# Performance work log

Hardware: AMD Instinct MI355X
Metric: run time of the kernel (lower is better)

Reference implementation:

```python
import jax, jax.numpy as jnp
import numpy as np

N = 50000
E = 800000
IN_CH = 128
HID = 32
HEADS = 4
OUT_CH = 64
NEG_SLOPE = 0.2


def _gat_conv(x, src, dst, W, att_src, att_dst, bias, heads, out_ch, concat):
    # x: [N, F_in]; W: [F_in, heads*out_ch]; att_*: [heads, out_ch]; bias: [heads*out_ch] or [out_ch]
    n = x.shape[0]
    h = (x @ W).reshape(n, heads, out_ch)                  # [N, H, C]
    a_src = jnp.einsum('nhc,hc->nh', h, att_src)           # [N, H]
    a_dst = jnp.einsum('nhc,hc->nh', h, att_dst)           # [N, H]
    alpha = jax.nn.leaky_relu(a_src[src] + a_dst[dst], NEG_SLOPE)  # [E, H]
    # segment softmax over edges grouped by destination node
    amax = jax.ops.segment_max(alpha, dst, num_segments=n)  # [N, H]
    ex = jnp.exp(alpha - amax[dst])
    denom = jax.ops.segment_sum(ex, dst, num_segments=n)    # [N, H]
    att = ex / (denom[dst] + 1e-16)                         # [E, H]
    msg = h[src] * att[:, :, None]                          # [E, H, C]
    out = jax.ops.segment_sum(msg, dst, num_segments=n)     # [N, H, C]
    out = out.reshape(n, heads * out_ch) if concat else out.mean(axis=1)
    return out + bias


def setup_inputs() -> dict:
    key = jax.random.key(0)
    ks = jax.random.split(key, 9)
    x = jax.random.normal(ks[0], (N, IN_CH), dtype=jnp.float32)
    edge_index = jax.random.randint(ks[1], (2, E), 0, N, dtype=jnp.int64)
    s = 1.0 / np.sqrt(IN_CH)
    W1 = jax.random.normal(ks[2], (IN_CH, HEADS * HID), dtype=jnp.float32) * s
    att_src1 = jax.random.normal(ks[3], (HEADS, HID), dtype=jnp.float32) * 0.1
    att_dst1 = jax.random.normal(ks[4], (HEADS, HID), dtype=jnp.float32) * 0.1
    b1 = jnp.zeros((HEADS * HID,), dtype=jnp.float32)
    s2 = 1.0 / np.sqrt(HEADS * HID)
    W2 = jax.random.normal(ks[5], (HEADS * HID, OUT_CH), dtype=jnp.float32) * s2
    att_src2 = jax.random.normal(ks[6], (1, OUT_CH), dtype=jnp.float32) * 0.1
    att_dst2 = jax.random.normal(ks[7], (1, OUT_CH), dtype=jnp.float32) * 0.1
    b2 = jnp.zeros((OUT_CH,), dtype=jnp.float32)
    return {"x": x, "edge_index": edge_index, "W1": W1, "att_src1": att_src1,
            "att_dst1": att_dst1, "b1": b1, "W2": W2, "att_src2": att_src2,
            "att_dst2": att_dst2, "b2": b2}


def reference(x, edge_index, W1, att_src1, att_dst1, b1, W2, att_src2, att_dst2, b2):
    n = x.shape[0]
    # add self loops (PyG GATConv default add_self_loops=True)
    loops = jnp.arange(n, dtype=edge_index.dtype)
    src = jnp.concatenate([edge_index[0], loops])
    dst = jnp.concatenate([edge_index[1], loops])
    h = _gat_conv(x, src, dst, W1, att_src1, att_dst1, b1, HEADS, HID, True)
    h = jax.nn.leaky_relu(h, NEG_SLOPE)
    # dropout p=0.6 is identity at eval
    out = _gat_conv(h, src, dst, W2, att_src2, att_dst2, b2, 1, OUT_CH, False)
    return out
```

## Files before the change

### kernel.cpp

```cpp
#include <hip/hip_runtime.h>
#include <hip/hip_fp16.h>

#define NNODES 50000
#define NEDGES 800000
#define NSLOPE 0.2f
#define NB2 782
#define BCAP2 1280
#define CSRB 256
#define EPB 3125
#define PAH 136

typedef _Float16 half8v __attribute__((ext_vector_type(8)));
typedef float floatx4 __attribute__((ext_vector_type(4)));

__device__ __forceinline__ float lrelu(float x) { return x > 0.f ? x : NSLOPE * x; }

__device__ __forceinline__ void fmamix8(float* acc, uint4 v, float w) {
    asm("v_fma_mix_f32 %0, %1, %2, %0 op_sel:[0,0,0] op_sel_hi:[0,1,0]" : "+v"(acc[0]) : "v"(w), "v"(v.x));
    asm("v_fma_mix_f32 %0, %1, %2, %0 op_sel:[0,1,0] op_sel_hi:[0,1,0]" : "+v"(acc[1]) : "v"(w), "v"(v.x));
    asm("v_fma_mix_f32 %0, %1, %2, %0 op_sel:[0,0,0] op_sel_hi:[0,1,0]" : "+v"(acc[2]) : "v"(w), "v"(v.y));
    asm("v_fma_mix_f32 %0, %1, %2, %0 op_sel:[0,1,0] op_sel_hi:[0,1,0]" : "+v"(acc[3]) : "v"(w), "v"(v.y));
    asm("v_fma_mix_f32 %0, %1, %2, %0 op_sel:[0,0,0] op_sel_hi:[0,1,0]" : "+v"(acc[4]) : "v"(w), "v"(v.z));
    asm("v_fma_mix_f32 %0, %1, %2, %0 op_sel:[0,1,0] op_sel_hi:[0,1,0]" : "+v"(acc[5]) : "v"(w), "v"(v.z));
    asm("v_fma_mix_f32 %0, %1, %2, %0 op_sel:[0,0,0] op_sel_hi:[0,1,0]" : "+v"(acc[6]) : "v"(w), "v"(v.w));
    asm("v_fma_mix_f32 %0, %1, %2, %0 op_sel:[0,1,0] op_sel_hi:[0,1,0]" : "+v"(acc[7]) : "v"(w), "v"(v.w));
}

__global__ __launch_bounds__(256) void wconv_kernel(const float* __restrict__ W1,
                                                    const float* __restrict__ W2,
                                                    __half* __restrict__ Wf1,
                                                    __half* __restrict__ Wf2) {
    int tid = blockIdx.x * 256 + threadIdx.x;
    if (tid < 2048) {
        int l = tid & 63, t = (tid >> 6) & 7, ks = tid >> 9;
        int col = t * 16 + (l & 15), kq = l >> 4;
        __half* dst = Wf1 + (size_t)tid * 8;
#pragma unroll
        for (int j = 0; j < 8; j++)
            dst[j] = __float2half(W1[(ks * 32 + kq * 8 + j) * 128 + col]);
    } else if (tid < 3072) {
        int u = tid - 2048;
        int l = u & 63, t = (u >> 6) & 3, ks = u >> 8;
        int col = t * 16 + (l & 15), kq = l >> 4;
        __half* dst = Wf2 + (size_t)u * 8;
#pragma unroll
        for (int j = 0; j < 8; j++)
            dst[j] = __float2half(W2[(ks * 32 + kq * 8 + j) * 64 + col]);
    }
}

template<int NCOL, int HEADS, typename AT>
__device__ void gemm_mfma_body(int bid, __half* __restrict__ Ah,
                               const AT* __restrict__ A, const __half* __restrict__ Wf,
                               const float* __restrict__ atts, const float* __restrict__ attd,
                               __half* __restrict__ H, float* __restrict__ as_,
                               float* __restrict__ ad_, int nrows) {
    constexpr int NT = NCOL / 16;
    constexpr int TPH = NT / HEADS;
    int t = threadIdx.x;
    long r0 = (long)bid * 64;
    long abase = r0 * 128, alimit = (long)nrows * 128;
#pragma unroll
    for (int i = 0; i < 8; i++) {
        int off = i * 1024 + t * 4;
        uint2 pk = make_uint2(0, 0);
        if (abase + off < alimit) {
            if constexpr (sizeof(AT) == 4) {
                float4 v = *(const float4*)&A[abase + off];
                __half2 h0 = __floats2half2_rn(v.x, v.y);
                __half2 h1 = __floats2half2_rn(v.z, v.w);
                pk = make_uint2(*(unsigned*)&h0, *(unsigned*)&h1);
            } else {
                pk = *(const uint2*)&A[abase + off];
            }
        }
        *(uint2*)&Ah[(off >> 7) * PAH + (off & 127)] = pk;
    }
    __syncthreads();

    int w = t >> 6, l = t & 63;
    int i16 = l & 15, q = l >> 4;
    floatx4 acc[NT];
#pragma unroll
    for (int n = 0; n < NT; n++) acc[n] = (floatx4)0.f;
    const half8v* wf = (const half8v*)Wf;
#pragma unroll
    for (int ks = 0; ks < 4; ks++) {
        half8v afrag = *(const half8v*)&Ah[(w * 16 + i16) * PAH + ks * 32 + q * 8];
#pragma unroll
        for (int n = 0; n < NT; n++) {
            half8v bfrag = wf[(ks * NT + n) * 64 + l];
            acc[n] = __builtin_amdgcn_mfma_f32_16x16x32_f16(afrag, bfrag, acc[n], 0, 0, 0);
        }
    }
    long rb = r0 + w * 16 + q * 4;
#pragma unroll
    for (int n = 0; n < NT; n++) {
#pragma unroll
        for (int reg = 0; reg < 4; reg++) {
            long row = rb + reg;
            if (row < nrows) H[row * NCOL + n * 16 + i16] = __float2half(acc[n][reg]);
        }
    }
    float ps[4][HEADS], pd[4][HEADS];
#pragma unroll
    for (int reg = 0; reg < 4; reg++)
#pragma unroll
        for (int h = 0; h < HEADS; h++) { ps[reg][h] = 0.f; pd[reg][h] = 0.f; }
#pragma unroll
    for (int n = 0; n < NT; n++) {
        float sa = atts[n * 16 + i16], da = attd[n * 16 + i16];
        int h = n / TPH;
#pragma unroll
        for (int reg = 0; reg < 4; reg++) {
            ps[reg][h] += acc[n][reg] * sa;
            pd[reg][h] += acc[n][reg] * da;
        }
    }
#pragma unroll
    for (int reg = 0; reg < 4; reg++)
#pragma unroll
        for (int h = 0; h < HEADS; h++)
#pragma unroll
            for (int m = 1; m < 16; m <<= 1) {
                ps[reg][h] += __shfl_xor(ps[reg][h], m);
                pd[reg][h] += __shfl_xor(pd[reg][h], m);
            }
    if (i16 < HEADS) {
        int h = i16;
#pragma unroll
        for (int reg = 0; reg < 4; reg++) {
            long row = rb + reg;
            if (row < nrows) {
                float pv = 0.f, dv = 0.f;
#pragma unroll
                for (int hh = 0; hh < HEADS; hh++) { if (hh == h) { pv = ps[reg][hh]; dv = pd[reg][hh]; } }
                as_[row * HEADS + h] = pv;
                ad_[row * HEADS + h] = dv;
            }
        }
    }
}

__global__ __launch_bounds__(256) void fused_csr_gemm1_kernel(
    const int* __restrict__ ei, unsigned* __restrict__ priv,
    int* __restrict__ cnt_mtx, int* __restrict__ lofs_mtx,
    const float* __restrict__ A, const __half* __restrict__ Wf1,
    const float* __restrict__ atts, const float* __restrict__ attd,
    __half* __restrict__ H, float* __restrict__ as_, float* __restrict__ ad_, int nrows) {
    __shared__ __align__(16) char smem[21760];
    if (blockIdx.x >= CSRB) {
        gemm_mfma_body<128, 4, float>(blockIdx.x - CSRB, (__half*)smem, A, Wf1, atts, attd,
                                      H, as_, ad_, nrows);
        return;
    }
    int* hist = (int*)smem;
    int* lofs = hist + 1024;
    int* sbuf = lofs + 1024;
    unsigned* ebuf = (unsigned*)(sbuf + 256);
    int tid = threadIdx.x;
    for (int i = tid; i < 1024; i += 256) hist[i] = 0;
    __syncthreads();
    int e0 = blockIdx.x * EPB;
    int dreg[13];
#pragma unroll
    for (int i = 0; i < 13; i++) {
        int e = e0 + i * 256 + tid;
        dreg[i] = (e < e0 + EPB) ? ei[NEDGES + e] : -1;
        if (dreg[i] >= 0) atomicAdd(&hist[dreg[i] >> 6], 1);
    }
    __syncthreads();
    int t4 = tid * 4;
    int a0 = hist[t4], a1 = hist[t4 + 1], a2 = hist[t4 + 2], a3 = hist[t4 + 3];
    int p1 = a0 + a1, p2 = p1 + a2, p3 = p2 + a3;
    sbuf[tid] = p3;
    __syncthreads();
    for (int off = 1; off < 256; off <<= 1) {
        int v = (tid >= off) ? sbuf[tid - off] : 0;
        __syncthreads();
        sbuf[tid] += v;
        __syncthreads();
    }
    int base = (tid > 0) ? sbuf[tid - 1] : 0;
    lofs[t4] = base; lofs[t4 + 1] = base + a0; lofs[t4 + 2] = base + p1; lofs[t4 + 3] = base + p2;
#pragma unroll
    for (int j = 0; j < 4; j++) {
        int i = t4 + j;
        if (i < NB2) {
            cnt_mtx[(long)blockIdx.x * NB2 + i] = hist[i];
            lofs_mtx[(long)blockIdx.x * NB2 + i] = lofs[i];
        }
    }
    hist[t4] = 0; hist[t4 + 1] = 0; hist[t4 + 2] = 0; hist[t4 + 3] = 0;
    __syncthreads();
#pragma unroll
    for (int i = 0; i < 13; i++) {
        if (dreg[i] >= 0) {
            int e = e0 + i * 256 + tid;
            int s = ei[e];
            int b = dreg[i] >> 6;
            int r = atomicAdd(&hist[b], 1);
            ebuf[lofs[b] + r] = (unsigned)s | ((unsigned)(dreg[i] & 63) << 16);
        }
    }
    __syncthreads();
    unsigned* seg = priv + (long)blockIdx.x * EPB;
    for (int i = tid; i < EPB; i += 256) seg[i] = ebuf[i];
}

__global__ __launch_bounds__(256) void consumer_kernel(
    const unsigned* __restrict__ priv, const int* __restrict__ cnt_mtx,
    const int* __restrict__ lofs_mtx, int* __restrict__ ssrc,
    int* __restrict__ offs, int* __restrict__ ends) {
    __shared__ int dcnt[64], dbase[64], dcur[64];
    __shared__ unsigned ebuf[BCAP2];
    int b = blockIdx.x, tid = threadIdx.x;
    if (tid < 64) dcnt[tid] = 0;
    int cnt = cnt_mtx[(long)tid * NB2 + b];
    int lof = lofs_mtx[(long)tid * NB2 + b];
    const unsigned* seg = priv + (long)tid * EPB + lof;
    __syncthreads();
    for (int k = 0; k < cnt; k++) {
        unsigned v = seg[k];
        atomicAdd(&dcnt[(v >> 16) & 63], 1);
    }
    __syncthreads();
    if (tid < 64) {
        int v = dcnt[tid], p = v;
#pragma unroll
        for (int off = 1; off < 64; off <<= 1) {
            int u = __shfl_up(p, off);
            if (tid >= off) p += u;
        }
        dbase[tid] = p - v;
        dcur[tid] = p - v;
    }
    __syncthreads();
    for (int k = 0; k < cnt; k++) {
        unsigned v = seg[k];
        int dl = (v >> 16) & 63;
        int r = atomicAdd(&dcur[dl], 1);
        if (r < BCAP2) ebuf[r] = v & 0xFFFFu;
    }
    __syncthreads();
    int obase = b * BCAP2;
    int n = dbase[63] + dcnt[63];
    if (n > BCAP2) n = BCAP2;
    for (int i = tid; i < n; i += 256) ssrc[obase + i] = (int)ebuf[i];
    if (tid < 64) {
        int d = b * 64 + tid;
        if (d < NNODES) {
            int s0 = dbase[tid], e1 = s0 + dcnt[tid];
            if (s0 > BCAP2) s0 = BCAP2;
            if (e1 > BCAP2) e1 = BCAP2;
            offs[d] = obase + s0;
            ends[d] = obase + e1;
        }
    }
}

template<int NCOL, int HEADS, typename AT>
__global__ __launch_bounds__(256) void gemm_att_kernel(
    const AT* __restrict__ A, const __half* __restrict__ Wf,
    const float* __restrict__ atts, const float* __restrict__ attd,
    __half* __restrict__ H, float* __restrict__ as_, float* __restrict__ ad_,
    int nrows) {
    __shared__ __align__(16) __half Ah[64 * PAH];
    gemm_mfma_body<NCOL, HEADS, AT>(blockIdx.x, Ah, A, Wf, atts, attd, H, as_, ad_, nrows);
}

template<int HEADS, int NCOL, int LRELU, typename OT>
__global__ __launch_bounds__(256) void gather_kernel(
    const int* __restrict__ ssrc, const int* __restrict__ offs,
    const int* __restrict__ ends, const float* __restrict__ as_,
    const float* __restrict__ ad_, const __half* __restrict__ H,
    const float* __restrict__ bias, OT* __restrict__ out, int n) {
    constexpr int CHUNK = 64 / HEADS;
    constexpr int LPE = NCOL / 8;
    constexpr int EPI = 64 / LPE;
    int wave = (blockIdx.x * blockDim.x + threadIdx.x) >> 6;
    if (wave >= n) return;
    int lane = threadIdx.x & 63;
    int d = wave;
    int sub = lane / LPE;
    int c = (lane % LPE) * 8;
    int hc = (HEADS == 1) ? 0 : (c >> 5);
    int SB = hc * CHUNK;
    int pe = (HEADS == 1) ? lane : (lane % CHUNK);
    int ph = (HEADS == 1) ? 0 : (lane / CHUNK);
    float ad_p = ad_[d * HEADS + ph];
    float acc[8];
#pragma unroll
    for (int i = 0; i < 8; i++) acc[i] = 0.f;
    float dsum = 0.f;
    int start = offs[d], end = ends[d];

    int base = start;
    int m = end - base; if (m > CHUNK) m = CHUNK;
    int sv = 0; float wv = 0.f;
    if (m > 0) {
        if (pe < m) {
            sv = ssrc[base + pe];
            wv = __expf(lrelu(as_[sv * HEADS + ph] + ad_p));
        }
        dsum += wv;
    }
    while (m > 0) {
        int nbase = base + CHUNK;
        int nm = end - nbase; if (nm > CHUNK) nm = CHUNK;
        int svn = 0;
        if (nm > 0 && pe < nm) svn = ssrc[nbase + pe];
        int i = 0;
        for (; i + 4 * EPI <= m; i += 4 * EPI) {
            int i0 = i + sub, i1 = i + EPI + sub, i2 = i + 2 * EPI + sub, i3 = i + 3 * EPI + sub;
            int s0 = __shfl(sv, SB + i0);
            int s1 = __shfl(sv, SB + i1);
            int s2 = __shfl(sv, SB + i2);
            int s3 = __shfl(sv, SB + i3);
            uint4 v0 = *(const uint4*)&H[(long)s0 * NCOL + c];
            uint4 v1 = *(const uint4*)&H[(long)s1 * NCOL + c];
            uint4 v2 = *(const uint4*)&H[(long)s2 * NCOL + c];
            uint4 v3 = *(const uint4*)&H[(long)s3 * NCOL + c];
            float w0 = __shfl(wv, SB + i0);
            float w1 = __shfl(wv, SB + i1);
            float w2 = __shfl(wv, SB + i2);
            float w3 = __shfl(wv, SB + i3);
            fmamix8(acc, v0, w0); fmamix8(acc, v1, w1);
            fmamix8(acc, v2, w2); fmamix8(acc, v3, w3);
        }
        for (; i < m; i += EPI) {
            int idx = i + sub;
            int cl = (idx < m) ? idx : (m - 1);
            int s = __shfl(sv, SB + cl);
            float w = __shfl(wv, SB + cl);
            if (idx >= m) w = 0.f;
            uint4 v = *(const uint4*)&H[(long)s * NCOL + c];
            fmamix8(acc, v, w);
        }
        if (nm <= 0) break;
        float wvn = 0.f;
        if (pe < nm) wvn = __expf(lrelu(as_[svn * HEADS + ph] + ad_p));
        dsum += wvn;
        sv = svn; wv = wvn; m = nm; base = nbase;
    }

    if (HEADS == 1) {
#pragma unroll
        for (int msk = 1; msk < 64; msk <<= 1) dsum += __shfl_xor(dsum, msk);
    } else {
#pragma unroll
        for (int msk = 1; msk < 16; msk <<= 1) dsum += __shfl_xor(dsum, msk);
        dsum = __shfl(dsum, SB);
    }
#pragma unroll
    for (int msk = LPE; msk < 64; msk <<= 1) {
#pragma unroll
        for (int i = 0; i < 8; i++) acc[i] += __shfl_xor(acc[i], msk);
    }
    {
        float wself = __expf(lrelu(as_[d * HEADS + hc] + ad_[d * HEADS + hc]));
        dsum += wself;
        uint4 vs = *(const uint4*)&H[(long)d * NCOL + c];
        fmamix8(acc, vs, wself);
    }
    float inv = 1.f / (dsum + 1e-16f);
    if (lane < LPE) {
        float r[8];
#pragma unroll
        for (int i = 0; i < 8; i++) {
            r[i] = acc[i] * inv + bias[c + i];
            if (LRELU) r[i] = lrelu(r[i]);
        }
        if constexpr (sizeof(OT) == 2) {
            __half2 q0 = __floats2half2_rn(r[0], r[1]);
            __half2 q1 = __floats2half2_rn(r[2], r[3]);
            __half2 q2 = __floats2half2_rn(r[4], r[5]);
            __half2 q3 = __floats2half2_rn(r[6], r[7]);
            uint4 pk = make_uint4(*(unsigned*)&q0, *(unsigned*)&q1, *(unsigned*)&q2, *(unsigned*)&q3);
            *(uint4*)&out[(long)d * NCOL + c] = pk;
        } else {
            *(float4*)&out[(long)d * NCOL + c] = make_float4(r[0], r[1], r[2], r[3]);
            *(float4*)&out[(long)d * NCOL + c + 4] = make_float4(r[4], r[5], r[6], r[7]);
        }
    }
}

static inline int nblk(long total) { return (int)((total + 255) / 256); }

extern "C" void kernel_launch(void* const* d_in, const int* in_sizes, int n_in,
                              void* d_out, int out_size, void* d_ws, size_t ws_size,
                              hipStream_t stream) {
    const float* x    = (const float*)d_in[0];
    const int*   ei   = (const int*)d_in[1];
    const float* W1   = (const float*)d_in[2];
    const float* as1w = (const float*)d_in[3];
    const float* ad1w = (const float*)d_in[4];
    const float* b1   = (const float*)d_in[5];
    const float* W2   = (const float*)d_in[6];
    const float* as2w = (const float*)d_in[7];
    const float* ad2w = (const float*)d_in[8];
    const float* b2   = (const float*)d_in[9];
    float* out = (float*)d_out;

    char* wsb = (char*)d_ws;
    size_t o = 0;
    __half* h1    = (__half*)(wsb + o); o += (size_t)NNODES * 128 * 2;
    __half* x2h   = (__half*)(wsb + o); o += (size_t)NNODES * 128 * 2;
    float* a_src1 = (float*)(wsb + o);  o += (size_t)NNODES * 4 * 4;
    float* a_dst1 = (float*)(wsb + o);  o += (size_t)NNODES * 4 * 4;
    float* a_src2 = (float*)(wsb + o);  o += (size_t)NNODES * 4;
    float* a_dst2 = (float*)(wsb + o);  o += (size_t)NNODES * 4;
    int* offs    = (int*)(wsb + o); o += (size_t)NNODES * 4;
    int* ends    = (int*)(wsb + o); o += (size_t)NNODES * 4;
    int* ssrc    = (int*)(wsb + o); o += (size_t)NB2 * BCAP2 * 4;
    unsigned* priv = (unsigned*)(wsb + o); o += (size_t)CSRB * EPB * 4;
    int* cnt_mtx  = (int*)(wsb + o); o += (size_t)CSRB * NB2 * 4;
    int* lofs_mtx = (int*)(wsb + o); o += (size_t)CSRB * NB2 * 4;
    __half* Wf1  = (__half*)(wsb + o); o += (size_t)2048 * 8 * 2;
    __half* Wf2  = (__half*)(wsb + o); o += (size_t)1024 * 8 * 2;
    __half* h2 = h1;

    const int GB = (NNODES + 63) / 64;

    wconv_kernel<<<12, 256, 0, stream>>>(W1, W2, Wf1, Wf2);

    fused_csr_gemm1_kernel<<<CSRB + GB, 256, 0, stream>>>(
        ei, priv, cnt_mtx, lofs_mtx, x, Wf1, as1w, ad1w, h1, a_src1, a_dst1, NNODES);
    consumer_kernel<<<NB2, 256, 0, stream>>>(priv, cnt_mtx, lofs_mtx, ssrc, offs, ends);

    gather_kernel<4, 128, 1, __half><<<nblk((long)NNODES * 64), 256, 0, stream>>>(
        ssrc, offs, ends, a_src1, a_dst1, h1, b1, x2h, NNODES);

    gemm_att_kernel<64, 1, __half><<<GB, 256, 0, stream>>>(
        x2h, Wf2, as2w, ad2w, h2, a_src2, a_dst2, NNODES);
    gather_kernel<1, 64, 0, float><<<nblk((long)NNODES * 64), 256, 0, stream>>>(
        ssrc, offs, ends, a_src2, a_dst2, h2, b2, out, NNODES);
}
```

Measured before the change: 120.9 us.

## Software-pipeline gather loads: prefetch next chunk's H rows into registers

Restructures the per-destination gather loop so the H feature rows for the next chunk of edges are loaded into a register buffer while the current chunk is accumulated. This double-buffers the random gathers to hide memory latency. In exchange it always issues NV loads per chunk, even when the chunk is partially full (clamped to duplicate rows), and it raises register pressure, which may reduce occupancy.

```diff
diff --git a/kernel.cpp b/kernel.cpp
--- a/kernel.cpp
+++ b/kernel.cpp
@@ -278,6 +278,7 @@
     constexpr int CHUNK = 64 / HEADS;
     constexpr int LPE = NCOL / 8;
     constexpr int EPI = 64 / LPE;
+    constexpr int NV = CHUNK / EPI;
     int wave = (blockIdx.x * blockDim.x + threadIdx.x) >> 6;
     if (wave >= n) return;
     int lane = threadIdx.x & 63;
@@ -298,50 +299,52 @@
     int base = start;
     int m = end - base; if (m > CHUNK) m = CHUNK;
     int sv = 0; float wv = 0.f;
+    uint4 vA[NV];
     if (m > 0) {
         if (pe < m) {
             sv = ssrc[base + pe];
             wv = __expf(lrelu(as_[sv * HEADS + ph] + ad_p));
         }
         dsum += wv;
+#pragma unroll
+        for (int k = 0; k < NV; k++) {
+            int idx = k * EPI + sub;
+            int cl = idx < m ? idx : m - 1;
+            int s = __shfl(sv, SB + cl);
+            vA[k] = *(const uint4*)&H[(long)s * NCOL + c];
+        }
     }
     while (m > 0) {
         int nbase = base + CHUNK;
         int nm = end - nbase; if (nm > CHUNK) nm = CHUNK;
-        int svn = 0;
-        if (nm > 0 && pe < nm) svn = ssrc[nbase + pe];
-        int i = 0;
-        for (; i + 4 * EPI <= m; i += 4 * EPI) {
-            int i0 = i + sub, i1 = i + EPI + sub, i2 = i + 2 * EPI + sub, i3 = i + 3 * EPI + sub;
-            int s0 = __shfl(sv, SB + i0);
-            int s1 = __shfl(sv, SB + i1);
-            int s2 = __shfl(sv, SB + i2);
-            int s3 = __shfl(sv, SB + i3);
-            uint4 v0 = *(const uint4*)&H[(long)s0 * NCOL + c];
-            uint4 v1 = *(const uint4*)&H[(long)s1 * NCOL + c];
-            uint4 v2 = *(const uint4*)&H[(long)s2 * NCOL + c];
-            uint4 v3 = *(const uint4*)&H[(long)s3 * NCOL + c];
-            float w0 = __shfl(wv, SB + i0);
-            float w1 = __shfl(wv, SB + i1);
-            float w2 = __shfl(wv, SB + i2);
-            float w3 = __shfl(wv, SB + i3);
-            fmamix8(acc, v0, w0); fmamix8(acc, v1, w1);
-            fmamix8(acc, v2, w2); fmamix8(acc, v3, w3);
-        }
-        for (; i < m; i += EPI) {
-            int idx = i + sub;
-            int cl = (idx < m) ? idx : (m - 1);
-            int s = __shfl(sv, SB + cl);
+        int svn = 0; float wvn = 0.f;
+        uint4 vB[NV];
+        if (nm > 0) {
+            if (pe < nm) {
+                svn = ssrc[nbase + pe];
+                wvn = __expf(lrelu(as_[svn * HEADS + ph] + ad_p));
+            }
+            dsum += wvn;
+#pragma unroll
+            for (int k = 0; k < NV; k++) {
+                int idx = k * EPI + sub;
+                int cl = idx < nm ? idx : nm - 1;
+                int s = __shfl(svn, SB + cl);
+                vB[k] = *(const uint4*)&H[(long)s * NCOL + c];
+            }
+        }
+#pragma unroll
+        for (int k = 0; k < NV; k++) {
+            int idx = k * EPI + sub;
+            int cl = idx < m ? idx : m - 1;
             float w = __shfl(wv, SB + cl);
             if (idx >= m) w = 0.f;
-            uint4 v = *(const uint4*)&H[(long)s * NCOL + c];
-            fmamix8(acc, v, w);
+            fmamix8(acc, vA[k], w);
         }
         if (nm <= 0) break;
-        float wvn = 0.f;
-        if (pe < nm) wvn = __expf(lrelu(as_[svn * HEADS + ph] + ad_p));
-        dsum += wvn;
         sv = svn; wv = wvn; m = nm; base = nbase;
+#pragma unroll
+        for (int k = 0; k < NV; k++) vA[k] = vB[k];
     }
 
     if (HEADS == 1) {
```

After: 131.7 us. +8.9%, slower.
